# Kernel optimization log

Measured on AMD Instinct MI355X. Metric: run time of the kernel, lower is better.

Reference implementation:

```python
import jax, jax.numpy as jnp
import numpy as np
from jax import lax

DIM = 64
HEADS = 4
B, Q, V = 8, 128, 128


def _modrelu(z, b):
    m = jnp.abs(z)
    return z * (jax.nn.relu(m + b) / (m + 1e-5))


def _eunn_unitary(h, th1, ph1, th2, ph2, om):
    # tunable-style EUNN, capacity 2: even-pair rotations, odd-pair rotations, diagonal phase
    d = h.shape[-1]
    # layer 1: pairs (0,1),(2,3),...
    hp = h.reshape(*h.shape[:-1], d // 2, 2)
    a, b = hp[..., 0], hp[..., 1]
    c1, s1, e1 = jnp.cos(th1), jnp.sin(th1), jnp.exp(1j * ph1)
    h = jnp.stack([e1 * (c1 * a - s1 * b), s1 * a + c1 * b], -1).reshape(h.shape)
    # layer 2: pairs (1,2),(3,4),...,(d-3,d-2); endpoints pass through
    mid = h[..., 1:d - 1].reshape(*h.shape[:-1], d // 2 - 1, 2)
    a, b = mid[..., 0], mid[..., 1]
    c2, s2, e2 = jnp.cos(th2), jnp.sin(th2), jnp.exp(1j * ph2)
    mid2 = jnp.stack([e2 * (c2 * a - s2 * b), s2 * a + c2 * b], -1).reshape(*h.shape[:-1], d - 2)
    h = jnp.concatenate([h[..., :1], mid2, h[..., d - 1:]], -1)
    return h * jnp.exp(1j * om)


def _forward(queries, values, U_re, U_im, bias, theta1, phi1, theta2, phi2, omega, W_dense, b_dense):
    Bq, Qq, d = queries.shape
    Vv = values.shape[1]
    # quadratic (query, value) expansion -> [B*Q, V, 2d]
    dq = jnp.broadcast_to(queries[:, :, None, :], (Bq, Qq, Vv, d))
    dv = jnp.broadcast_to(values[:, None, :, :], (Bq, Qq, Vv, d))
    x = jnp.concatenate([dq, dv], -1).reshape(Bq * Qq, Vv, 2 * d)
    U = (U_re + 1j * U_im)  # [H, 2d, d] complex input kernel per head
    Ux = jnp.einsum('nvi,hij->hvnj', x.astype(jnp.complex64), U)  # [H, V, N, d]

    def run_head(Ux_h, t1, p1, t2, p2, om, bh):
        def step(h, u):
            h2 = _modrelu(_eunn_unitary(h, t1, p1, t2, p2, om) + u, bh)
            return h2, None
        h0 = jnp.zeros(Ux_h.shape[1:], dtype=jnp.complex64)  # [N, d]
        hT, _ = lax.scan(step, h0, Ux_h)
        return hT  # final state, as Keras RNN with return_sequences=False

    outs = jax.vmap(run_head)(Ux, theta1, phi1, theta2, phi2, omega, bias)  # [H, N, d]
    acc = jnp.real(outs).transpose(1, 0, 2).reshape(Bq * Qq, HEADS * d)
    y = acc @ W_dense + b_dense
    return y.reshape(Bq, Qq, d)


def setup_inputs() -> dict:
    key = jax.random.key(0)
    ks = jax.random.split(key, 12)
    pi = np.pi
    return {
        'queries': jax.random.normal(ks[0], (B, Q, DIM), jnp.float32),
        'values': jax.random.normal(ks[1], (B, V, DIM), jnp.float32),
        'U_re': jax.random.normal(ks[2], (HEADS, 2 * DIM, DIM), jnp.float32) * (1.0 / np.sqrt(2 * DIM)),
        'U_im': jax.random.normal(ks[3], (HEADS, 2 * DIM, DIM), jnp.float32) * (1.0 / np.sqrt(2 * DIM)),
        'bias': jax.random.normal(ks[4], (HEADS, DIM), jnp.float32) * 0.01,
        'theta1': jax.random.uniform(ks[5], (HEADS, DIM // 2), jnp.float32, -pi, pi),
        'phi1': jax.random.uniform(ks[6], (HEADS, DIM // 2), jnp.float32, -pi, pi),
        'theta2': jax.random.uniform(ks[7], (HEADS, DIM // 2 - 1), jnp.float32, -pi, pi),
        'phi2': jax.random.uniform(ks[8], (HEADS, DIM // 2 - 1), jnp.float32, -pi, pi),
        'omega': jax.random.uniform(ks[9], (HEADS, DIM), jnp.float32, -pi, pi),
        'W_dense': jax.random.normal(ks[10], (HEADS * DIM, DIM), jnp.float32) * (1.0 / np.sqrt(HEADS * DIM)),
        'b_dense': jnp.zeros((DIM,), jnp.float32),
    }


def reference(queries, values, U_re, U_im, bias, theta1, phi1, theta2, phi2, omega, W_dense, b_dense):
    return _forward(queries, values, U_re, U_im, bias, theta1, phi1, theta2, phi2, omega, W_dense, b_dense)
```

## Files before the change

### kernel.cpp

```cpp
#include <hip/hip_runtime.h>
#include <math.h>

#define DIM 64
#define HEADS 4
#define BB 8
#define QQ 128
#define VV 128
#define NN (BB*QQ)

typedef float f2 __attribute__((ext_vector_type(2)));

__device__ __forceinline__ float dpp_swap1(float x) {
    return __int_as_float(__builtin_amdgcn_update_dpp(
        0, __float_as_int(x), 0xB1, 0xF, 0xF, true));
}
__device__ __forceinline__ float dpp_wshr1(float x) {
    return __int_as_float(__builtin_amdgcn_update_dpp(
        0, __float_as_int(x), 0x138, 0xF, 0xF, true));
}
__device__ __forceinline__ float dpp_wshl1(float x) {
    return __int_as_float(__builtin_amdgcn_update_dpp(
        0, __float_as_int(x), 0x130, 0xF, 0xF, true));
}

__global__ __launch_bounds__(256) void k_av(const float* __restrict__ values,
                                            const float* __restrict__ U_re,
                                            const float* __restrict__ U_im,
                                            f2* __restrict__ Av) {
    int tid = blockIdx.x * blockDim.x + threadIdx.x;
    int w = tid >> 6;
    int j = tid & 63;
    int h = w >> 8;
    int r0 = (w & 255) << 2;
    const float* vrow = values + r0 * DIM;
    const float* ur = U_re + (h * 2 * DIM + DIM) * DIM + j;
    const float* ui = U_im + (h * 2 * DIM + DIM) * DIM + j;
    f2 a0 = 0.f, a1 = 0.f, a2 = 0.f, a3 = 0.f;
    #pragma unroll 8
    for (int i = 0; i < DIM; ++i) {
        f2 u; u.x = ur[i * DIM]; u.y = ui[i * DIM];
        a0 += vrow[i] * u;
        a1 += vrow[DIM + i] * u;
        a2 += vrow[2 * DIM + i] * u;
        a3 += vrow[3 * DIM + i] * u;
    }
    f2* out = Av + (h * 1024 + r0) * DIM + j;
    out[0] = a0; out[DIM] = a1; out[2 * DIM] = a2; out[3 * DIM] = a3;
}

__global__ __launch_bounds__(256, 4) void k_rnn_dense(
        const float* __restrict__ queries,
        const float* __restrict__ U_re,
        const float* __restrict__ U_im,
        const float* __restrict__ bias,
        const float* __restrict__ theta1,
        const float* __restrict__ phi1,
        const float* __restrict__ theta2,
        const float* __restrict__ phi2,
        const float* __restrict__ omega,
        const f2* __restrict__ Av,
        const float* __restrict__ W_dense,
        const float* __restrict__ b_dense,
        float* __restrict__ y) {
    int n = blockIdx.x;
    int t = threadIdx.x;
    int h = t >> 6;
    int j = t & 63;
    int b = n >> 7;

    int k1 = j >> 1;
    float th1 = theta1[h * 32 + k1], ph1 = phi1[h * 32 + k1];
    float c1 = cosf(th1), s1 = sinf(th1);
    float A1r, A1i, B1r, B1i;
    if ((j & 1) == 0) {
        float er = cosf(ph1), ei = sinf(ph1);
        A1r = er * c1; A1i = ei * c1;
        B1r = -er * s1; B1i = -ei * s1;
    } else {
        A1r = c1; A1i = 0.f;
        B1r = s1; B1i = 0.f;
    }

    float A2r, A2i, BLr, BLi, BRr, BRi;
    if (j == 0 || j == 63) {
        A2r = 1.f; A2i = 0.f; BLr = 0.f; BLi = 0.f; BRr = 0.f; BRi = 0.f;
    } else {
        int k2 = (j - 1) >> 1;
        float th2 = theta2[h * 31 + k2], ph2 = phi2[h * 31 + k2];
        float c2 = cosf(th2), s2 = sinf(th2);
        if (j & 1) {
            float er = cosf(ph2), ei = sinf(ph2);
            A2r = er * c2; A2i = ei * c2;
            BLr = -er * s2; BLi = -ei * s2;
            BRr = 0.f; BRi = 0.f;
        } else {
            A2r = c2; A2i = 0.f;
            BRr = s2; BRi = 0.f;
            BLr = 0.f; BLi = 0.f;
        }
    }
    {
        float om = omega[h * 64 + j];
        float eor = cosf(om), eoi = sinf(om);
        float tr, ti;
        tr = A2r * eor - A2i * eoi; ti = A2r * eoi + A2i * eor; A2r = tr; A2i = ti;
        tr = BLr * eor - BLi * eoi; ti = BLr * eoi + BLi * eor; BLr = tr; BLi = ti;
        tr = BRr * eor - BRi * eoi; ti = BRr * eoi + BRi * eor; BRr = tr; BRi = ti;
    }
    float bj = bias[h * 64 + j];

    const float* qrow = queries + n * DIM;
    const float* ur = U_re + (h * 2 * DIM) * DIM + j;
    const float* ui = U_im + (h * 2 * DIM) * DIM + j;
    float uqr = 0.f, uqi = 0.f;
    #pragma unroll 8
    for (int i = 0; i < DIM; ++i) {
        float a = qrow[i];
        uqr = fmaf(a, ur[i * DIM], uqr);
        uqi = fmaf(a, ui[i * DIM], uqi);
    }

    const f2* Avp = Av + (h * 1024 + b * 128) * DIM + j;

    float hr = 0.f, hi = 0.f;
    f2 av0 = Avp[0];
    float uvr = uqr + av0.x, uvi = uqi + av0.y;
    f2 avn = Avp[DIM];
    #pragma unroll 4
    for (int v = 0; v < VV; ++v) {
        f2 av2 = Avp[((v + 2) & 127) * DIM];
        float pr = dpp_swap1(hr), pi = dpp_swap1(hi);
        float t_r = (A1r * hr - A1i * hi) + (B1r * pr - B1i * pi);
        float t_i = (A1r * hi + A1i * hr) + (B1r * pi + B1i * pr);
        float Lr = dpp_wshl1(t_r), Li = dpp_wshl1(t_i);
        float Rr = dpp_wshr1(t_r), Ri = dpp_wshr1(t_i);
        float s_r = (A2r * t_r - A2i * t_i) + (BLr * Lr - BLi * Li) + (BRr * Rr - BRi * Ri);
        float s_i = (A2r * t_i + A2i * t_r) + (BLr * Li + BLi * Lr) + (BRr * Ri + BRi * Rr);
        float zr = s_r + uvr;
        float zi = s_i + uvi;
        uvr = uqr + avn.x; uvi = uqi + avn.y;
        avn = av2;
        float q2 = fmaf(zr, zr, fmaf(zi, zi, 1e-10f));
        float rs = __builtin_amdgcn_rsqf(q2);
        float tp = fmaxf(fmaf(q2, rs, bj), 0.f);
        float sc = tp * rs;
        hr = zr * sc; hi = zi * sc;
    }

    __shared__ float s_acc[HEADS * DIM];
    __shared__ float s_part[256];
    s_acc[h * 64 + j] = hr;
    __syncthreads();

    {
        int qq = t >> 6, jj = t & 63;
        const float* Wp = W_dense + (qq * 64) * DIM + jj;
        const float* ap = &s_acc[qq * 64];
        float part = 0.f;
        #pragma unroll 8
        for (int k = 0; k < 64; ++k)
            part = fmaf(ap[k], Wp[k * DIM], part);
        s_part[t] = part;
    }
    __syncthreads();
    if (t < 64) {
        y[n * DIM + t] = b_dense[t] + s_part[t] + s_part[64 + t]
                       + s_part[128 + t] + s_part[192 + t];
    }
}

extern "C" void kernel_launch(void* const* d_in, const int* in_sizes, int n_in,
                              void* d_out, int out_size, void* d_ws, size_t ws_size,
                              hipStream_t stream) {
    const float* queries = (const float*)d_in[0];
    const float* values  = (const float*)d_in[1];
    const float* U_re    = (const float*)d_in[2];
    const float* U_im    = (const float*)d_in[3];
    const float* bias    = (const float*)d_in[4];
    const float* theta1  = (const float*)d_in[5];
    const float* phi1    = (const float*)d_in[6];
    const float* theta2  = (const float*)d_in[7];
    const float* phi2    = (const float*)d_in[8];
    const float* omega   = (const float*)d_in[9];
    const float* W_dense = (const float*)d_in[10];
    const float* b_dense = (const float*)d_in[11];
    float* y = (float*)d_out;

    f2* Av = (f2*)d_ws;

    k_av<<<256, 256, 0, stream>>>(values, U_re, U_im, Av);
    k_rnn_dense<<<1024, 256, 0, stream>>>(queries, U_re, U_im, bias, theta1,
                                          phi1, theta2, phi2, omega, Av,
                                          W_dense, b_dense, y);
}
```

Before: 131.5 us.

## Factor EUNN rotations into real cos/sin plus phase, prefetch Av in blocks

```diff
diff --git a/kernel.cpp b/kernel.cpp
--- a/kernel.cpp
+++ b/kernel.cpp
@@ -10,18 +10,14 @@
 
 typedef float f2 __attribute__((ext_vector_type(2)));
 
-__device__ __forceinline__ float dpp_swap1(float x) {
+template <int CTRL>
+__device__ __forceinline__ float dppf(float x) {
     return __int_as_float(__builtin_amdgcn_update_dpp(
-        0, __float_as_int(x), 0xB1, 0xF, 0xF, true));
+        0, __float_as_int(x), CTRL, 0xF, 0xF, true));
 }
-__device__ __forceinline__ float dpp_wshr1(float x) {
-    return __int_as_float(__builtin_amdgcn_update_dpp(
-        0, __float_as_int(x), 0x138, 0xF, 0xF, true));
-}
-__device__ __forceinline__ float dpp_wshl1(float x) {
-    return __int_as_float(__builtin_amdgcn_update_dpp(
-        0, __float_as_int(x), 0x130, 0xF, 0xF, true));
-}
+#define SWAP1 0xB1
+#define WSHR1 0x138
+#define WSHL1 0x130
 
 __global__ __launch_bounds__(256) void k_av(const float* __restrict__ values,
                                             const float* __restrict__ U_re,
@@ -30,22 +26,20 @@
     int tid = blockIdx.x * blockDim.x + threadIdx.x;
     int w = tid >> 6;
     int j = tid & 63;
-    int h = w >> 8;
-    int r0 = (w & 255) << 2;
+    int h = w >> 9;
+    int r0 = (w & 511) << 1;
     const float* vrow = values + r0 * DIM;
     const float* ur = U_re + (h * 2 * DIM + DIM) * DIM + j;
     const float* ui = U_im + (h * 2 * DIM + DIM) * DIM + j;
-    f2 a0 = 0.f, a1 = 0.f, a2 = 0.f, a3 = 0.f;
+    f2 a0 = 0.f, a1 = 0.f;
     #pragma unroll 8
     for (int i = 0; i < DIM; ++i) {
         f2 u; u.x = ur[i * DIM]; u.y = ui[i * DIM];
         a0 += vrow[i] * u;
         a1 += vrow[DIM + i] * u;
-        a2 += vrow[2 * DIM + i] * u;
-        a3 += vrow[3 * DIM + i] * u;
     }
     f2* out = Av + (h * 1024 + r0) * DIM + j;
-    out[0] = a0; out[DIM] = a1; out[2 * DIM] = a2; out[3 * DIM] = a3;
+    out[0] = a0; out[DIM] = a1;
 }
 
 __global__ __launch_bounds__(256, 4) void k_rnn_dense(
@@ -70,43 +64,25 @@
 
     int k1 = j >> 1;
     float th1 = theta1[h * 32 + k1], ph1 = phi1[h * 32 + k1];
-    float c1 = cosf(th1), s1 = sinf(th1);
-    float A1r, A1i, B1r, B1i;
-    if ((j & 1) == 0) {
-        float er = cosf(ph1), ei = sinf(ph1);
-        A1r = er * c1; A1i = ei * c1;
-        B1r = -er * s1; B1i = -ei * s1;
-    } else {
-        A1r = c1; A1i = 0.f;
-        B1r = s1; B1i = 0.f;
-    }
+    float C1 = cosf(th1), s1v = sinf(th1);
+    float S1, E1r, E1i;
+    if ((j & 1) == 0) { S1 = -s1v; E1r = cosf(ph1); E1i = sinf(ph1); }
+    else              { S1 =  s1v; E1r = 1.f;       E1i = 0.f;       }
 
-    float A2r, A2i, BLr, BLi, BRr, BRi;
+    float C2, SL, SR, p2r, p2i;
     if (j == 0 || j == 63) {
-        A2r = 1.f; A2i = 0.f; BLr = 0.f; BLi = 0.f; BRr = 0.f; BRi = 0.f;
+        C2 = 1.f; SL = 0.f; SR = 0.f; p2r = 1.f; p2i = 0.f;
     } else {
         int k2 = (j - 1) >> 1;
         float th2 = theta2[h * 31 + k2], ph2 = phi2[h * 31 + k2];
         float c2 = cosf(th2), s2 = sinf(th2);
-        if (j & 1) {
-            float er = cosf(ph2), ei = sinf(ph2);
-            A2r = er * c2; A2i = ei * c2;
-            BLr = -er * s2; BLi = -ei * s2;
-            BRr = 0.f; BRi = 0.f;
-        } else {
-            A2r = c2; A2i = 0.f;
-            BRr = s2; BRi = 0.f;
-            BLr = 0.f; BLi = 0.f;
-        }
+        if (j & 1) { C2 = c2; SL = -s2; SR = 0.f; p2r = cosf(ph2); p2i = sinf(ph2); }
+        else       { C2 = c2; SR =  s2; SL = 0.f; p2r = 1.f;       p2i = 0.f;       }
     }
-    {
-        float om = omega[h * 64 + j];
-        float eor = cosf(om), eoi = sinf(om);
-        float tr, ti;
-        tr = A2r * eor - A2i * eoi; ti = A2r * eoi + A2i * eor; A2r = tr; A2i = ti;
-        tr = BLr * eor - BLi * eoi; ti = BLr * eoi + BLi * eor; BLr = tr; BLi = ti;
-        tr = BRr * eor - BRi * eoi; ti = BRr * eoi + BRi * eor; BRr = tr; BRi = ti;
-    }
+    float om = omega[h * 64 + j];
+    float eor = cosf(om), eoi = sinf(om);
+    float PHr = p2r * eor - p2i * eoi;
+    float PHi = p2r * eoi + p2i * eor;
     float bj = bias[h * 64 + j];
 
     const float* qrow = queries + n * DIM;
@@ -120,31 +96,42 @@
         uqi = fmaf(a, ui[i * DIM], uqi);
     }
 
-    const f2* Avp = Av + (h * 1024 + b * 128) * DIM + j;
-
     float hr = 0.f, hi = 0.f;
-    f2 av0 = Avp[0];
-    float uvr = uqr + av0.x, uvi = uqi + av0.y;
-    f2 avn = Avp[DIM];
-    #pragma unroll 4
-    for (int v = 0; v < VV; ++v) {
-        f2 av2 = Avp[((v + 2) & 127) * DIM];
-        float pr = dpp_swap1(hr), pi = dpp_swap1(hi);
-        float t_r = (A1r * hr - A1i * hi) + (B1r * pr - B1i * pi);
-        float t_i = (A1r * hi + A1i * hr) + (B1r * pi + B1i * pr);
-        float Lr = dpp_wshl1(t_r), Li = dpp_wshl1(t_i);
-        float Rr = dpp_wshr1(t_r), Ri = dpp_wshr1(t_i);
-        float s_r = (A2r * t_r - A2i * t_i) + (BLr * Lr - BLi * Li) + (BRr * Rr - BRi * Ri);
-        float s_i = (A2r * t_i + A2i * t_r) + (BLr * Li + BLi * Lr) + (BRr * Ri + BRi * Rr);
-        float zr = s_r + uvr;
-        float zi = s_i + uvi;
-        uvr = uqr + avn.x; uvi = uqi + avn.y;
-        avn = av2;
+    auto step = [&](f2 av) {
+        float uvr = uqr + av.x;
+        float uvi = uqi + av.y;
+        float pr = dppf<SWAP1>(hr), pi = dppf<SWAP1>(hi);
+        float tpr = fmaf(C1, hr, S1 * pr);
+        float tpi = fmaf(C1, hi, S1 * pi);
+        float Tr = fmaf(E1r, tpr, -E1i * tpi);
+        float Ti = fmaf(E1r, tpi,  E1i * tpr);
+        float Lr = dppf<WSHL1>(Tr), Li = dppf<WSHL1>(Ti);
+        float Rr = dppf<WSHR1>(Tr), Ri = dppf<WSHR1>(Ti);
+        float spr = fmaf(C2, Tr, fmaf(SL, Lr, SR * Rr));
+        float spi = fmaf(C2, Ti, fmaf(SL, Li, SR * Ri));
+        float zr = fmaf(PHr, spr, fmaf(-PHi, spi, uvr));
+        float zi = fmaf(PHr, spi, fmaf( PHi, spr, uvi));
         float q2 = fmaf(zr, zr, fmaf(zi, zi, 1e-10f));
         float rs = __builtin_amdgcn_rsqf(q2);
-        float tp = fmaxf(fmaf(q2, rs, bj), 0.f);
-        float sc = tp * rs;
+        float sc = fmaxf(fmaf(bj, rs, 1.f), 0.f);
         hr = zr * sc; hi = zi * sc;
+    };
+
+    const f2* p = Av + (h * 1024 + b * 128) * DIM + j;
+
+    f2 buf[8], nxt[8];
+    #pragma unroll
+    for (int k = 0; k < 8; ++k) buf[k] = p[k * DIM];
+
+    for (int vb = 0; vb < VV; vb += 8) {
+        const f2* pn = p + ((vb < VV - 8) ? 8 * DIM : 0);
+        #pragma unroll
+        for (int k = 0; k < 8; ++k) nxt[k] = pn[k * DIM];
+        p = pn;
+        #pragma unroll
+        for (int k = 0; k < 8; ++k) step(buf[k]);
+        #pragma unroll
+        for (int k = 0; k < 8; ++k) buf[k] = nxt[k];
     }
 
     __shared__ float s_acc[HEADS * DIM];
@@ -188,7 +175,7 @@
 
     f2* Av = (f2*)d_ws;
 
-    k_av<<<256, 256, 0, stream>>>(values, U_re, U_im, Av);
+    k_av<<<512, 256, 0, stream>>>(values, U_re, U_im, Av);
     k_rnn_dense<<<1024, 256, 0, stream>>>(queries, U_re, U_im, bias, theta1,
                                           phi1, theta2, phi2, omega, Av,
                                           W_dense, b_dense, y);
```

Result: faster. 113.5 us (-13.7%).
